# Optimization experiments

Measured on AMD Instinct MI355X. Metric: run time of the kernel, lower is better.

Reference implementation:

```python
import jax, jax.numpy as jnp
import numpy as np

R = 3  # correlation radius -> (2R+1)^2 = 49 offsets
OFFSETS = [(dy, dx) for dy in range(-R, R + 1) for dx in range(-R, R + 1)]


def local_correlation(f1, f2):
    # f1, f2: [B, C, H, W] -> [B, 49, H, W]
    C = f1.shape[1]
    scale = np.float32(1.0 / np.sqrt(C))
    vols = [jnp.sum(f1 * jnp.roll(f2, (dy, dx), axis=(2, 3)), axis=1)
            for dy, dx in OFFSETS]  # fixed 49-offset structural loop
    return jnp.stack(vols, axis=1) * scale


def _level(lvl, w, b):
    # lvl: [T, B, C, H, W]; correlate consecutive frame pairs
    corr = jax.vmap(local_correlation)(lvl[:-1], lvl[1:])  # [T-1, B, 49, H, W]
    # 1x1 conv == channel contraction: [49, token_dim]
    return jnp.einsum('tbkhw,kd->tbdhw', corr, w) + b[None, None, :, None, None]


def setup_inputs() -> dict:
    key = jax.random.key(0)
    ks = jax.random.split(key, 9)
    T, B = 3, 2
    token_dim, K = 192, 49
    return {
        'l1': jax.random.normal(ks[0], (T, B, 64, 128, 128), jnp.float32),
        'l2': jax.random.normal(ks[1], (T, B, 128, 64, 64), jnp.float32),
        'l3': jax.random.normal(ks[2], (T, B, 192, 32, 32), jnp.float32),
        'w1': jax.random.normal(ks[3], (K, token_dim), jnp.float32) * 0.05,
        'b1': jax.random.normal(ks[4], (token_dim,), jnp.float32) * 0.05,
        'w2': jax.random.normal(ks[5], (K, token_dim), jnp.float32) * 0.05,
        'b2': jax.random.normal(ks[6], (token_dim,), jnp.float32) * 0.05,
        'w3': jax.random.normal(ks[7], (K, token_dim), jnp.float32) * 0.05,
        'b3': jax.random.normal(ks[8], (token_dim,), jnp.float32) * 0.05,
    }


def reference(l1, l2, l3, w1, b1, w2, b2, w3, b3):
    tok1 = _level(l1, w1, b1)  # [T-1, B, 192, 128, 128]
    tok2 = _level(l2, w2, b2)  # [T-1, B, 192, 64, 64]
    tok3 = _level(l3, w3, b3)  # [T-1, B, 192, 32, 32]
    return (tok1, tok2, tok3)
```

## Files before the change

kernel.cpp:

```cpp
#include <hip/hip_runtime.h>


#define TD 192

template<int C, int H, int W>
__device__ __forceinline__ void level_tile(
    const float* __restrict__ lvl, const float* __restrict__ wm,
    const float* __restrict__ bias, float* __restrict__ out,
    int pair, int tY, int tX, float scale,
    float4* __restrict__ hs, float* __restrict__ sc)
{
    const int HW = H * W;
    const int t  = pair >> 1, bb = pair & 1;
    const float* f1 = lvl + (t * 2 + bb) * C * HW;
    const float* f2 = lvl + ((t + 1) * 2 + bb) * C * HW;

    const int tid  = threadIdx.x;
    const int lane = tid & 63;
    const int g    = tid >> 6;
    const int tx   = lane & 15, ty = lane >> 4;
    const int x0   = tX * 16, y0 = tY * 4;
    const int x    = x0 + tx,  y  = y0 + ty;

    float4* h = hs + g * 230;

    int goff[4], loff[4];
#pragma unroll
    for (int i = 0; i < 4; ++i) {
        int p = lane + i * 64;
        int r = p / 22, cc = p - r * 22;
        int gy = y0 - 3 + r;  if (gy < 0) gy += H;  if (gy >= H) gy -= H;
        int gx = x0 - 3 + cc; if (gx < 0) gx += W;  if (gx >= W) gx -= W;
        goff[i] = gy * W + gx;
        loff[i] = r * 23 + cc;
    }

    float acc[49];
#pragma unroll
    for (int k = 0; k < 49; ++k) acc[k] = 0.f;

    const int NCH = C / 16;
    const float* f2c = f2 + g * (C / 4) * HW;
    const float* f1c = f1 + g * (C / 4) * HW + y * W + x;
#pragma unroll 1
    for (int cg = 0; cg < NCH; ++cg) {
#pragma unroll
        for (int i = 0; i < 4; ++i) {
            if (i < 3 || lane < 28) {
                const float* s = f2c + goff[i];
                float4 v; v.x = s[0]; v.y = s[HW]; v.z = s[2 * HW]; v.w = s[3 * HW];
                h[loff[i]] = v;
            }
        }
        float a0 = f1c[0], a1 = f1c[HW], a2 = f1c[2 * HW], a3 = f1c[3 * HW];
        f2c += 4 * HW; f1c += 4 * HW;
#pragma unroll
        for (int a = 0; a < 7; ++a) {
#pragma unroll
            for (int b = 0; b < 7; ++b) {
                float4 v = h[(ty + 6 - a) * 23 + (tx + 6 - b)];
                float s = acc[a * 7 + b];
                s = fmaf(a0, v.x, s);
                s = fmaf(a1, v.y, s);
                s = fmaf(a2, v.z, s);
                s = fmaf(a3, v.w, s);
                acc[a * 7 + b] = s;
            }
        }
    }

    float* s0 = sc;
    float* s1 = sc + 49 * 64;
    if (g >= 2) {
        float* dst = (g == 2) ? s0 : s1;
#pragma unroll
        for (int k = 0; k < 49; ++k) dst[k * 64 + lane] = acc[k];
    }
    __syncthreads();
    if (g < 2) {
        float* dst = (g == 0) ? s0 : s1;
#pragma unroll
        for (int k = 0; k < 49; ++k) dst[k * 64 + lane] += acc[k];
    }
    __syncthreads();

    const int dbase = __builtin_amdgcn_readfirstlane(g * 48);
    float sacc[48];
#pragma unroll
    for (int j = 0; j < 48; ++j) sacc[j] = bias[dbase + j];
#pragma unroll 1
    for (int k = 0; k < 49; ++k) {
        float c = (s0[k * 64 + lane] + s1[k * 64 + lane]) * scale;
        const float* wr = wm + k * TD + dbase;
#pragma unroll
        for (int j = 0; j < 48; ++j) sacc[j] = fmaf(wr[j], c, sacc[j]);
    }
    float* op = out + (pair * TD + dbase) * HW + y * W + x;
#pragma unroll
    for (int j = 0; j < 48; ++j) op[j * HW] = sacc[j];
}

__global__ __launch_bounds__(256, 2)
void cost_tokenizer(const float* __restrict__ l1, const float* __restrict__ l2,
                    const float* __restrict__ l3,
                    const float* __restrict__ w1, const float* __restrict__ b1,
                    const float* __restrict__ w2, const float* __restrict__ b2,
                    const float* __restrict__ w3, const float* __restrict__ b3,
                    float* __restrict__ out)
{
    __shared__ float4 hs[4 * 230];
    __shared__ float  sc[2 * 49 * 64];
    int bid = blockIdx.x;
    if (bid < 64) {
        int r = bid;
        level_tile<192, 32, 32>(l3, w3, b3, out + 15728640,
                                r >> 4, (r >> 1) & 7, r & 1,
                                0.072168783648703216f, hs, sc);
    } else if (bid < 320) {
        int r = bid - 64;
        level_tile<128, 64, 64>(l2, w2, b2, out + 12582912,
                                r >> 6, (r >> 2) & 15, r & 3,
                                0.088388347648318447f, hs, sc);
    } else {
        int r = bid - 320;
        level_tile<64, 128, 128>(l1, w1, b1, out,
                                 r >> 8, (r >> 3) & 31, r & 7,
                                 0.125f, hs, sc);
    }
}

extern "C" void kernel_launch(void* const* d_in, const int* in_sizes, int n_in,
                              void* d_out, int out_size, void* d_ws, size_t ws_size,
                              hipStream_t stream)
{
    const float* l1 = (const float*)d_in[0];
    const float* l2 = (const float*)d_in[1];
    const float* l3 = (const float*)d_in[2];
    const float* w1 = (const float*)d_in[3];
    const float* b1 = (const float*)d_in[4];
    const float* w2 = (const float*)d_in[5];
    const float* b2 = (const float*)d_in[6];
    const float* w3 = (const float*)d_in[7];
    const float* b3 = (const float*)d_in[8];
    float* out = (float*)d_out;

    hipLaunchKernelGGL(cost_tokenizer, dim3(1344), dim3(256), 0, stream,
                       l1, l2, l3, w1, b1, w2, b2, w3, b3, out);
}
```

Measured before the change: 161.0 us.

## Compute two output rows per thread and remap blocks for XCD locality

Each thread now produces two vertically adjacent output pixels. The tile grows to 16x8, so the halo is loaded once for twice the outputs and each LDS float4 read feeds both accumulators across the 7 row offsets. The grid is halved, block indices are remapped so neighbouring tiles land on the same XCD, shared memory is merged into one buffer, and the launch bound moves to 3 waves per EU. Doubling the accumulators and projection registers (98 plus 96 floats) risks register spills or lower occupancy, and halving the grid leaves fewer blocks to cover the load imbalance.

```diff
diff --git a/kernel.cpp b/kernel.cpp
--- a/kernel.cpp
+++ b/kernel.cpp
@@ -3,14 +3,18 @@
 
 #define TD 192
 
-template<int C, int H, int W>
+template<int C, int H, int W, int TX, int TY>
 __device__ __forceinline__ void level_tile(
     const float* __restrict__ lvl, const float* __restrict__ wm,
     const float* __restrict__ bias, float* __restrict__ out,
-    int pair, int tY, int tX, float scale,
-    float4* __restrict__ hs, float* __restrict__ sc)
+    int r, float scale, float* __restrict__ smem)
 {
     const int HW = H * W;
+    const int xcd = r & 7, q = r >> 3;
+    const int tY  = q % TY;
+    const int col = (q / TY) * 8 + xcd;
+    const int pair = col / TX, tX = col % TX;
+
     const int t  = pair >> 1, bb = pair & 1;
     const float* f1 = lvl + (t * 2 + bb) * C * HW;
     const float* f2 = lvl + ((t + 1) * 2 + bb) * C * HW;
@@ -18,26 +22,27 @@
     const int tid  = threadIdx.x;
     const int lane = tid & 63;
     const int g    = tid >> 6;
-    const int tx   = lane & 15, ty = lane >> 4;
-    const int x0   = tX * 16, y0 = tY * 4;
-    const int x    = x0 + tx,  y  = y0 + ty;
+    const int tx   = lane & 15, tyy = lane >> 4;
+    const int x0   = tX * 16, y0 = tY * 8;
+    const int x    = x0 + tx;
+    const int y    = y0 + 2 * tyy;
 
-    float4* h = hs + g * 230;
+    float4* h = (float4*)smem + g * 322;
 
-    int goff[4], loff[4];
+    int goff[5], loff[5];
 #pragma unroll
-    for (int i = 0; i < 4; ++i) {
+    for (int i = 0; i < 5; ++i) {
         int p = lane + i * 64;
-        int r = p / 22, cc = p - r * 22;
-        int gy = y0 - 3 + r;  if (gy < 0) gy += H;  if (gy >= H) gy -= H;
-        int gx = x0 - 3 + cc; if (gx < 0) gx += W;  if (gx >= W) gx -= W;
+        int rr = p / 22, cc = p - rr * 22;
+        int gy = y0 - 3 + rr; if (gy < 0) gy += H; if (gy >= H) gy -= H;
+        int gx = x0 - 3 + cc; if (gx < 0) gx += W; if (gx >= W) gx -= W;
         goff[i] = gy * W + gx;
-        loff[i] = r * 23 + cc;
+        loff[i] = rr * 23 + cc;
     }
 
-    float acc[49];
+    float acc0[49], acc1[49];
 #pragma unroll
-    for (int k = 0; k < 49; ++k) acc[k] = 0.f;
+    for (int k = 0; k < 49; ++k) { acc0[k] = 0.f; acc1[k] = 0.f; }
 
     const int NCH = C / 16;
     const float* f2c = f2 + g * (C / 4) * HW;
@@ -45,62 +50,79 @@
 #pragma unroll 1
     for (int cg = 0; cg < NCH; ++cg) {
 #pragma unroll
-        for (int i = 0; i < 4; ++i) {
-            if (i < 3 || lane < 28) {
+        for (int i = 0; i < 5; ++i) {
+            if (i < 4 || lane < 52) {
                 const float* s = f2c + goff[i];
                 float4 v; v.x = s[0]; v.y = s[HW]; v.z = s[2 * HW]; v.w = s[3 * HW];
                 h[loff[i]] = v;
             }
         }
-        float a0 = f1c[0], a1 = f1c[HW], a2 = f1c[2 * HW], a3 = f1c[3 * HW];
+        float a00 = f1c[0], a01 = f1c[HW], a02 = f1c[2 * HW], a03 = f1c[3 * HW];
+        float a10 = f1c[W], a11 = f1c[HW + W], a12 = f1c[2 * HW + W], a13 = f1c[3 * HW + W];
         f2c += 4 * HW; f1c += 4 * HW;
+#pragma unroll 1
+        for (int b = 0; b < 7; ++b) {
+            const float4* hp = h + (2 * tyy) * 23 + (tx + 6 - b);
+            float4 v[8];
 #pragma unroll
-        for (int a = 0; a < 7; ++a) {
+            for (int j = 0; j < 8; ++j) v[j] = hp[j * 23];
 #pragma unroll
-            for (int b = 0; b < 7; ++b) {
-                float4 v = h[(ty + 6 - a) * 23 + (tx + 6 - b)];
-                float s = acc[a * 7 + b];
-                s = fmaf(a0, v.x, s);
-                s = fmaf(a1, v.y, s);
-                s = fmaf(a2, v.z, s);
-                s = fmaf(a3, v.w, s);
-                acc[a * 7 + b] = s;
+            for (int a = 0; a < 7; ++a) {
+                float4 u0 = v[6 - a], u1 = v[7 - a];
+                float s0 = acc0[a * 7 + b], s1 = acc1[a * 7 + b];
+                s0 = fmaf(a00, u0.x, s0); s0 = fmaf(a01, u0.y, s0);
+                s0 = fmaf(a02, u0.z, s0); s0 = fmaf(a03, u0.w, s0);
+                s1 = fmaf(a10, u1.x, s1); s1 = fmaf(a11, u1.y, s1);
+                s1 = fmaf(a12, u1.z, s1); s1 = fmaf(a13, u1.w, s1);
+                acc0[a * 7 + b] = s0; acc1[a * 7 + b] = s1;
             }
         }
     }
 
-    float* s0 = sc;
-    float* s1 = sc + 49 * 64;
+    __syncthreads();
+    float* s0p = smem;
+    float* s1p = smem + 49 * 128;
     if (g >= 2) {
-        float* dst = (g == 2) ? s0 : s1;
-#pragma unroll
-        for (int k = 0; k < 49; ++k) dst[k * 64 + lane] = acc[k];
+        float* dst = (g == 2) ? s0p : s1p;
+#pragma unroll 1
+        for (int k = 0; k < 49; ++k) {
+            dst[k * 128 + lane]      = acc0[k];
+            dst[k * 128 + 64 + lane] = acc1[k];
+        }
     }
     __syncthreads();
     if (g < 2) {
-        float* dst = (g == 0) ? s0 : s1;
-#pragma unroll
-        for (int k = 0; k < 49; ++k) dst[k * 64 + lane] += acc[k];
+        float* dst = (g == 0) ? s0p : s1p;
+#pragma unroll 1
+        for (int k = 0; k < 49; ++k) {
+            dst[k * 128 + lane]      += acc0[k];
+            dst[k * 128 + 64 + lane] += acc1[k];
+        }
     }
     __syncthreads();
 
     const int dbase = __builtin_amdgcn_readfirstlane(g * 48);
-    float sacc[48];
+    float sA[48], sB[48];
 #pragma unroll
-    for (int j = 0; j < 48; ++j) sacc[j] = bias[dbase + j];
+    for (int j = 0; j < 48; ++j) { float bv = bias[dbase + j]; sA[j] = bv; sB[j] = bv; }
 #pragma unroll 1
     for (int k = 0; k < 49; ++k) {
-        float c = (s0[k * 64 + lane] + s1[k * 64 + lane]) * scale;
+        float c0 = (s0p[k * 128 + lane]      + s1p[k * 128 + lane])      * scale;
+        float c1 = (s0p[k * 128 + 64 + lane] + s1p[k * 128 + 64 + lane]) * scale;
         const float* wr = wm + k * TD + dbase;
 #pragma unroll
-        for (int j = 0; j < 48; ++j) sacc[j] = fmaf(wr[j], c, sacc[j]);
+        for (int j = 0; j < 48; ++j) {
+            float wv = wr[j];
+            sA[j] = fmaf(wv, c0, sA[j]);
+            sB[j] = fmaf(wv, c1, sB[j]);
+        }
     }
     float* op = out + (pair * TD + dbase) * HW + y * W + x;
-#pragma unroll
-    for (int j = 0; j < 48; ++j) op[j * HW] = sacc[j];
+#pragma unroll 1
+    for (int j = 0; j < 48; ++j) { op[j * HW] = sA[j]; op[j * HW + W] = sB[j]; }
 }
 
-__global__ __launch_bounds__(256, 2)
+__global__ __launch_bounds__(256, 3)
 void cost_tokenizer(const float* __restrict__ l1, const float* __restrict__ l2,
                     const float* __restrict__ l3,
                     const float* __restrict__ w1, const float* __restrict__ b1,
@@ -108,24 +130,17 @@
                     const float* __restrict__ w3, const float* __restrict__ b3,
                     float* __restrict__ out)
 {
-    __shared__ float4 hs[4 * 230];
-    __shared__ float  sc[2 * 49 * 64];
+    __shared__ __align__(16) float smem[12544];
     int bid = blockIdx.x;
-    if (bid < 64) {
-        int r = bid;
-        level_tile<192, 32, 32>(l3, w3, b3, out + 15728640,
-                                r >> 4, (r >> 1) & 7, r & 1,
-                                0.072168783648703216f, hs, sc);
-    } else if (bid < 320) {
-        int r = bid - 64;
-        level_tile<128, 64, 64>(l2, w2, b2, out + 12582912,
-                                r >> 6, (r >> 2) & 15, r & 3,
-                                0.088388347648318447f, hs, sc);
+    if (bid < 32) {
+        level_tile<192, 32, 32, 2, 4>(l3, w3, b3, out + 15728640,
+                                      bid, 0.072168783648703216f, smem);
+    } else if (bid < 160) {
+        level_tile<128, 64, 64, 4, 8>(l2, w2, b2, out + 12582912,
+                                      bid - 32, 0.088388347648318447f, smem);
     } else {
-        int r = bid - 320;
-        level_tile<64, 128, 128>(l1, w1, b1, out,
-                                 r >> 8, (r >> 3) & 31, r & 7,
-                                 0.125f, hs, sc);
+        level_tile<64, 128, 128, 8, 16>(l1, w1, b1, out,
+                                        bid - 160, 0.125f, smem);
     }
 }
 
@@ -144,6 +159,6 @@
     const float* b3 = (const float*)d_in[8];
     float* out = (float*)d_out;
 
-    hipLaunchKernelGGL(cost_tokenizer, dim3(1344), dim3(256), 0, stream,
+    hipLaunchKernelGGL(cost_tokenizer, dim3(672), dim3(256), 0, stream,
                        l1, l2, l3, w1, b1, w2, b2, w3, b3, out);
 }
```

Result: slower. 342.5 us (+112.8%).
